# Optimization experiments

Hardware: AMD Instinct MI355X
Metric: run time of the kernel (lower is better)

Reference implementation:

```python
import jax, jax.numpy as jnp
import numpy as np

N_NODES = 100000
N_EDGES = 625000
D_IN = 128
D_OUT = 128


def setup_inputs() -> dict:
    key = jax.random.key(0)
    k1, k2, k3, k4, k5 = jax.random.split(key, 5)
    feature = jax.random.normal(k1, (N_NODES, D_IN), dtype=jnp.float32)
    W = jax.random.normal(k2, (D_OUT, D_IN), dtype=jnp.float32) * (1.0 / np.sqrt(D_IN))
    b = jax.random.normal(k3, (D_OUT,), dtype=jnp.float32) * 0.01
    src = jax.random.randint(k4, (N_EDGES,), 0, N_NODES, dtype=jnp.int64)
    dst = jax.random.randint(k5, (N_EDGES,), 0, N_NODES, dtype=jnp.int64)
    return {"feature": feature, "W": W, "b": b, "src": src, "dst": dst}


def reference(feature, W, b, src, dst):
    # copy_src: gather source-node features along edges -> [E, D_IN]
    msg = feature[src]
    # mean reduce over incoming edges per destination node
    agg = jax.ops.segment_sum(msg, dst, num_segments=N_NODES)  # [N, D_IN]
    deg = jax.ops.segment_sum(jnp.ones((dst.shape[0],), feature.dtype), dst,
                              num_segments=N_NODES)  # [N]
    # DGL mean leaves nodes with zero in-degree at 0
    h = jnp.where(deg[:, None] > 0, agg / jnp.maximum(deg, 1.0)[:, None], 0.0)
    # nn.Linear: h @ W.T + b
    return h @ W.T + b
```

## Files before the change

### kernel.cpp

```cpp
#include <hip/hip_runtime.h>

#define D 128
#define CAP 32

typedef __attribute__((ext_vector_type(8))) short short8;
typedef __attribute__((ext_vector_type(4))) float f32x4;

__device__ __forceinline__ unsigned short f2bf_rne(float x) {
    unsigned int u = __float_as_uint(x);
    u += 0x7fffu + ((u >> 16) & 1u);
    return (unsigned short)(u >> 16);
}

__global__ __launch_bounds__(256)
void pack_all(const float* __restrict__ feat, const float* __restrict__ W,
              ushort* __restrict__ fb, ushort* __restrict__ Wb, int n4) {
    int i = blockIdx.x * 256 + threadIdx.x;
    if (i < n4) {
        float4 v = ((const float4*)feat)[i];
        ushort4 o;
        o.x = f2bf_rne(v.x); o.y = f2bf_rne(v.y);
        o.z = f2bf_rne(v.z); o.w = f2bf_rne(v.w);
        ((ushort4*)fb)[i] = o;
    } else if (i < n4 + 32) {
        ((ushort4*)fb)[i] = make_ushort4(0, 0, 0, 0);
    } else if (i < n4 + 32 + 4096) {
        int j = i - (n4 + 32);
        float4 v = ((const float4*)W)[j];
        ushort4 o;
        o.x = f2bf_rne(v.x); o.y = f2bf_rne(v.y);
        o.z = f2bf_rne(v.z); o.w = f2bf_rne(v.w);
        ((ushort4*)Wb)[j] = o;
    }
}

__global__ __launch_bounds__(256)
void build_buckets(const int* __restrict__ src,
                   const int* __restrict__ dst,
                   int* __restrict__ cnt,
                   int* __restrict__ bucket,
                   int n_edges) {
    int e = blockIdx.x * 256 + threadIdx.x;
    if (e >= n_edges) return;
    int d = dst[e];
    int p = atomicAdd(cnt + d, 1);
    if (p < CAP) bucket[(size_t)d * CAP + p] = src[e];
}

__global__ __launch_bounds__(256)
void agg_gemm(const ushort* __restrict__ fb,
              const int* __restrict__ cnt,
              const int* __restrict__ bucket,
              const ushort* __restrict__ Wb,
              const float* __restrict__ b,
              float* __restrict__ out,
              int n_nodes) {
    __shared__ ushort hs[32 * 136];
    int t = threadIdx.x;
    int lane = t & 63;
    int wave = t >> 6;
    int nb = blockIdx.x * 32;
    int base = nb + wave * 8;

    int myc = (lane < 8) ? cnt[base + lane] : 0;

    const ushort* fbl = fb + (size_t)(lane << 1);

    for (int g = 0; g < 2; ++g) {
        int n0g = base + g * 4;
        int nA = n0g + (lane >> 5);
        int nB = n0g + 2 + (lane >> 5);
        int idsA = bucket[(size_t)nA * CAP + (lane & 31)];
        int idsB = bucket[(size_t)nB * CAP + (lane & 31)];
        int d0 = __shfl(myc, g * 4 + 0);
        int d1 = __shfl(myc, g * 4 + 1);
        int d2 = __shfl(myc, g * 4 + 2);
        int d3 = __shfl(myc, g * 4 + 3);
        int m0 = d0 < CAP ? d0 : CAP;
        int m1 = d1 < CAP ? d1 : CAP;
        int m2 = d2 < CAP ? d2 : CAP;
        int m3 = d3 < CAP ? d3 : CAP;
        int mA = (lane < 32) ? m0 : m1;
        int mB = (lane < 32) ? m2 : m3;
        idsA = ((lane & 31) < mA) ? idsA : n_nodes;
        idsB = ((lane & 31) < mB) ? idsB : n_nodes;
        int mm01 = m0 > m1 ? m0 : m1;
        int mm23 = m2 > m3 ? m2 : m3;
        int mmax = mm01 > mm23 ? mm01 : mm23;

        float ax0 = 0, ay0 = 0, ax1 = 0, ay1 = 0;
        float ax2 = 0, ay2 = 0, ax3 = 0, ay3 = 0;

        for (int j = 0; j < mmax; j += 8) {
            unsigned int v0[8], v1[8], v2[8], v3[8];
#pragma unroll
            for (int i = 0; i < 8; ++i) {
                int s0 = __shfl(idsA, j + i);
                int s1 = __shfl(idsA, 32 + j + i);
                int s2 = __shfl(idsB, j + i);
                int s3 = __shfl(idsB, 32 + j + i);
                v0[i] = *(const unsigned int*)(fbl + (size_t)s0 * D);
                v1[i] = *(const unsigned int*)(fbl + (size_t)s1 * D);
                v2[i] = *(const unsigned int*)(fbl + (size_t)s2 * D);
                v3[i] = *(const unsigned int*)(fbl + (size_t)s3 * D);
            }
#pragma unroll
            for (int i = 0; i < 8; ++i) {
                ax0 += __uint_as_float(v0[i] << 16); ay0 += __uint_as_float(v0[i] & 0xffff0000u);
                ax1 += __uint_as_float(v1[i] << 16); ay1 += __uint_as_float(v1[i] & 0xffff0000u);
                ax2 += __uint_as_float(v2[i] << 16); ay2 += __uint_as_float(v2[i] & 0xffff0000u);
                ax3 += __uint_as_float(v3[i] << 16); ay3 += __uint_as_float(v3[i] & 0xffff0000u);
            }
        }

        float i0 = d0 > 0 ? 1.0f / (float)d0 : 0.0f;
        float i1 = d1 > 0 ? 1.0f / (float)d1 : 0.0f;
        float i2 = d2 > 0 ? 1.0f / (float)d2 : 0.0f;
        float i3 = d3 > 0 ? 1.0f / (float)d3 : 0.0f;
        unsigned int* hsu = (unsigned int*)hs;
        int r0 = wave * 8 + g * 4;
        hsu[(r0 + 0) * 68 + lane] = ((unsigned int)f2bf_rne(ay0 * i0) << 16) | f2bf_rne(ax0 * i0);
        hsu[(r0 + 1) * 68 + lane] = ((unsigned int)f2bf_rne(ay1 * i1) << 16) | f2bf_rne(ax1 * i1);
        hsu[(r0 + 2) * 68 + lane] = ((unsigned int)f2bf_rne(ay2 * i2) << 16) | f2bf_rne(ax2 * i2);
        hsu[(r0 + 3) * 68 + lane] = ((unsigned int)f2bf_rne(ay3 * i3) << 16) | f2bf_rne(ax3 * i3);
    }
    __syncthreads();

    int mt = wave & 1;
    int nh = wave >> 1;
    int lane16 = lane & 15;
    int lq = lane >> 4;

    f32x4 acc[4] = {{0,0,0,0},{0,0,0,0},{0,0,0,0},{0,0,0,0}};
#pragma unroll
    for (int ks = 0; ks < 4; ++ks) {
        short8 afrg = *(const short8*)&hs[(mt * 16 + lane16) * 136 + ks * 32 + lq * 8];
#pragma unroll
        for (int tt = 0; tt < 4; ++tt) {
            short8 bfrg = *(const short8*)&Wb[(size_t)(nh * 64 + tt * 16 + lane16) * D + ks * 32 + lq * 8];
            acc[tt] = __builtin_amdgcn_mfma_f32_16x16x32_bf16(afrg, bfrg, acc[tt], 0, 0, 0);
        }
    }

#pragma unroll
    for (int tt = 0; tt < 4; ++tt) {
        int o = nh * 64 + tt * 16 + lane16;
        float bb = b[o];
        int node = nb + mt * 16 + lq * 4;
#pragma unroll
        for (int r = 0; r < 4; ++r) {
            out[(size_t)(node + r) * D + o] = acc[tt][r] + bb;
        }
    }
}

extern "C" void kernel_launch(void* const* d_in, const int* in_sizes, int n_in,
                              void* d_out, int out_size, void* d_ws, size_t ws_size,
                              hipStream_t stream) {
    const float* feat = (const float*)d_in[0];
    const float* W    = (const float*)d_in[1];
    const float* bia  = (const float*)d_in[2];
    const int* src = (const int*)d_in[3];
    const int* dst = (const int*)d_in[4];
    float* out = (float*)d_out;

    int n_nodes = in_sizes[0] / D;
    int n_edges = in_sizes[3];

    size_t off = 0;
    auto alloc = [&](size_t bytes) { size_t p = off; off = (off + bytes + 4095) & ~(size_t)4095; return p; };
    size_t cnt_off    = alloc((size_t)n_nodes * sizeof(int));
    size_t bucket_off = alloc((size_t)n_nodes * CAP * sizeof(int));
    size_t wb_off     = alloc((size_t)D * D * sizeof(ushort));
    size_t fb_off     = alloc((size_t)(n_nodes + 1) * D * sizeof(ushort));

    int*    cnt    = (int*)((char*)d_ws + cnt_off);
    int*    bucket = (int*)((char*)d_ws + bucket_off);
    ushort* Wb     = (ushort*)((char*)d_ws + wb_off);
    ushort* fb     = (ushort*)((char*)d_ws + fb_off);

    int n4 = n_nodes * (D / 4);
    int G  = n4 + 32 + (D * D / 4);

    hipMemsetAsync(cnt, 0, (size_t)n_nodes * sizeof(int), stream);
    pack_all<<<(G + 255) / 256, 256, 0, stream>>>(feat, W, fb, Wb, n4);
    build_buckets<<<(n_edges + 255) / 256, 256, 0, stream>>>(src, dst, cnt, bucket, n_edges);
    agg_gemm<<<n_nodes / 32, 256, 0, stream>>>(fb, cnt, bucket, Wb, bia, out, n_nodes);
}
```

Measured before the change: 190.7 us.

## Fuse pack and bucket kernels; gather 8 nodes per wave with 8-byte loads

Merges the bf16 packing kernel and the edge-bucketing kernel into one launch, with a block-index split between the two jobs. This removes one kernel launch and lets the two memory-bound phases overlap. The aggregation loop is reorganised so each half-wave handles four nodes at once over all 8 nodes per wave. Each lane now loads 8 bytes (4 bf16) per neighbour instead of 4, halving the gather instructions, and the results are written to shared memory as uint2. The cost is more accumulator registers, and all 8 nodes in a wave now iterate to the wave's maximum degree instead of the maximum of each group of 4.

```diff
diff --git a/kernel.cpp b/kernel.cpp
--- a/kernel.cpp
+++ b/kernel.cpp
@@ -12,10 +12,27 @@
     return (unsigned short)(u >> 16);
 }
 
+__device__ __forceinline__ unsigned int pack_bf2(float x, float y) {
+    return ((unsigned int)f2bf_rne(y) << 16) | (unsigned int)f2bf_rne(x);
+}
+
 __global__ __launch_bounds__(256)
-void pack_all(const float* __restrict__ feat, const float* __restrict__ W,
-              ushort* __restrict__ fb, ushort* __restrict__ Wb, int n4) {
-    int i = blockIdx.x * 256 + threadIdx.x;
+void pack_build(const float* __restrict__ feat, const float* __restrict__ W,
+                ushort* __restrict__ fb, ushort* __restrict__ Wb,
+                const int* __restrict__ src, const int* __restrict__ dst,
+                int* __restrict__ cnt, int* __restrict__ bucket,
+                int n4, int n_edges, int edgeBlocks) {
+    int bx = blockIdx.x;
+    if (bx < edgeBlocks) {
+        int e = bx * 256 + threadIdx.x;
+        if (e < n_edges) {
+            int d = dst[e];
+            int p = atomicAdd(cnt + d, 1);
+            if (p < CAP) bucket[(size_t)d * CAP + p] = src[e];
+        }
+        return;
+    }
+    int i = (bx - edgeBlocks) * 256 + threadIdx.x;
     if (i < n4) {
         float4 v = ((const float4*)feat)[i];
         ushort4 o;
@@ -35,19 +52,6 @@
 }
 
 __global__ __launch_bounds__(256)
-void build_buckets(const int* __restrict__ src,
-                   const int* __restrict__ dst,
-                   int* __restrict__ cnt,
-                   int* __restrict__ bucket,
-                   int n_edges) {
-    int e = blockIdx.x * 256 + threadIdx.x;
-    if (e >= n_edges) return;
-    int d = dst[e];
-    int p = atomicAdd(cnt + d, 1);
-    if (p < CAP) bucket[(size_t)d * CAP + p] = src[e];
-}
-
-__global__ __launch_bounds__(256)
 void agg_gemm(const ushort* __restrict__ fb,
               const int* __restrict__ cnt,
               const int* __restrict__ bucket,
@@ -62,68 +66,90 @@
     int nb = blockIdx.x * 32;
     int base = nb + wave * 8;
 
+    int hi = lane >> 5;
+    int l31 = lane & 31;
+    int half32 = lane & 32;
+
     int myc = (lane < 8) ? cnt[base + lane] : 0;
 
-    const ushort* fbl = fb + (size_t)(lane << 1);
-
-    for (int g = 0; g < 2; ++g) {
-        int n0g = base + g * 4;
-        int nA = n0g + (lane >> 5);
-        int nB = n0g + 2 + (lane >> 5);
-        int idsA = bucket[(size_t)nA * CAP + (lane & 31)];
-        int idsB = bucket[(size_t)nB * CAP + (lane & 31)];
-        int d0 = __shfl(myc, g * 4 + 0);
-        int d1 = __shfl(myc, g * 4 + 1);
-        int d2 = __shfl(myc, g * 4 + 2);
-        int d3 = __shfl(myc, g * 4 + 3);
-        int m0 = d0 < CAP ? d0 : CAP;
-        int m1 = d1 < CAP ? d1 : CAP;
-        int m2 = d2 < CAP ? d2 : CAP;
-        int m3 = d3 < CAP ? d3 : CAP;
-        int mA = (lane < 32) ? m0 : m1;
-        int mB = (lane < 32) ? m2 : m3;
-        idsA = ((lane & 31) < mA) ? idsA : n_nodes;
-        idsB = ((lane & 31) < mB) ? idsB : n_nodes;
-        int mm01 = m0 > m1 ? m0 : m1;
-        int mm23 = m2 > m3 ? m2 : m3;
-        int mmax = mm01 > mm23 ? mm01 : mm23;
-
-        float ax0 = 0, ay0 = 0, ax1 = 0, ay1 = 0;
-        float ax2 = 0, ay2 = 0, ax3 = 0, ay3 = 0;
-
-        for (int j = 0; j < mmax; j += 8) {
-            unsigned int v0[8], v1[8], v2[8], v3[8];
-#pragma unroll
-            for (int i = 0; i < 8; ++i) {
-                int s0 = __shfl(idsA, j + i);
-                int s1 = __shfl(idsA, 32 + j + i);
-                int s2 = __shfl(idsB, j + i);
-                int s3 = __shfl(idsB, 32 + j + i);
-                v0[i] = *(const unsigned int*)(fbl + (size_t)s0 * D);
-                v1[i] = *(const unsigned int*)(fbl + (size_t)s1 * D);
-                v2[i] = *(const unsigned int*)(fbl + (size_t)s2 * D);
-                v3[i] = *(const unsigned int*)(fbl + (size_t)s3 * D);
-            }
-#pragma unroll
-            for (int i = 0; i < 8; ++i) {
-                ax0 += __uint_as_float(v0[i] << 16); ay0 += __uint_as_float(v0[i] & 0xffff0000u);
-                ax1 += __uint_as_float(v1[i] << 16); ay1 += __uint_as_float(v1[i] & 0xffff0000u);
-                ax2 += __uint_as_float(v2[i] << 16); ay2 += __uint_as_float(v2[i] & 0xffff0000u);
-                ax3 += __uint_as_float(v3[i] << 16); ay3 += __uint_as_float(v3[i] & 0xffff0000u);
-            }
-        }
-
-        float i0 = d0 > 0 ? 1.0f / (float)d0 : 0.0f;
-        float i1 = d1 > 0 ? 1.0f / (float)d1 : 0.0f;
-        float i2 = d2 > 0 ? 1.0f / (float)d2 : 0.0f;
-        float i3 = d3 > 0 ? 1.0f / (float)d3 : 0.0f;
-        unsigned int* hsu = (unsigned int*)hs;
-        int r0 = wave * 8 + g * 4;
-        hsu[(r0 + 0) * 68 + lane] = ((unsigned int)f2bf_rne(ay0 * i0) << 16) | f2bf_rne(ax0 * i0);
-        hsu[(r0 + 1) * 68 + lane] = ((unsigned int)f2bf_rne(ay1 * i1) << 16) | f2bf_rne(ax1 * i1);
-        hsu[(r0 + 2) * 68 + lane] = ((unsigned int)f2bf_rne(ay2 * i2) << 16) | f2bf_rne(ax2 * i2);
-        hsu[(r0 + 3) * 68 + lane] = ((unsigned int)f2bf_rne(ay3 * i3) << 16) | f2bf_rne(ax3 * i3);
-    }
+    unsigned int so = ((unsigned int)hi << 7) + (unsigned int)l31;
+    const int* bkt = bucket + (size_t)base * CAP;
+    int ids0 = bkt[ 0 + so];
+    int ids1 = bkt[32 + so];
+    int ids2 = bkt[64 + so];
+    int ids3 = bkt[96 + so];
+
+    int d0 = __shfl(myc, 0), d1 = __shfl(myc, 1), d2 = __shfl(myc, 2), d3 = __shfl(myc, 3);
+    int d4 = __shfl(myc, 4), d5 = __shfl(myc, 5), d6 = __shfl(myc, 6), d7 = __shfl(myc, 7);
+    int c0 = min(d0, CAP), c1 = min(d1, CAP), c2 = min(d2, CAP), c3 = min(d3, CAP);
+    int c4 = min(d4, CAP), c5 = min(d5, CAP), c6 = min(d6, CAP), c7 = min(d7, CAP);
+
+    int ms0 = hi ? c4 : c0;
+    int ms1 = hi ? c5 : c1;
+    int ms2 = hi ? c6 : c2;
+    int ms3 = hi ? c7 : c3;
+    ids0 = (l31 < ms0) ? ids0 : n_nodes;
+    ids1 = (l31 < ms1) ? ids1 : n_nodes;
+    ids2 = (l31 < ms2) ? ids2 : n_nodes;
+    ids3 = (l31 < ms3) ? ids3 : n_nodes;
+
+    int mm01 = c0 > c1 ? c0 : c1;
+    int mm23 = c2 > c3 ? c2 : c3;
+    int mm45 = c4 > c5 ? c4 : c5;
+    int mm67 = c6 > c7 ? c6 : c7;
+    int mmA = mm01 > mm23 ? mm01 : mm23;
+    int mmB = mm45 > mm67 ? mm45 : mm67;
+    int mmax = mmA > mmB ? mmA : mmB;
+
+    float a00=0,a01=0,a02=0,a03=0;
+    float a10=0,a11=0,a12=0,a13=0;
+    float a20=0,a21=0,a22=0,a23=0;
+    float a30=0,a31=0,a32=0,a33=0;
+
+    const char* fbb = (const char*)fb;
+    unsigned int colb = (unsigned int)l31 * 8u;
+
+    for (int j = 0; j < mmax; j += 4) {
+        uint2 v0[4], v1[4], v2[4], v3[4];
+#pragma unroll
+        for (int i = 0; i < 4; ++i) {
+            int sl = half32 + j + i;
+            unsigned int r0 = (unsigned int)__shfl(ids0, sl);
+            unsigned int r1 = (unsigned int)__shfl(ids1, sl);
+            unsigned int r2 = (unsigned int)__shfl(ids2, sl);
+            unsigned int r3 = (unsigned int)__shfl(ids3, sl);
+            v0[i] = *(const uint2*)(fbb + ((r0 << 8) + colb));
+            v1[i] = *(const uint2*)(fbb + ((r1 << 8) + colb));
+            v2[i] = *(const uint2*)(fbb + ((r2 << 8) + colb));
+            v3[i] = *(const uint2*)(fbb + ((r3 << 8) + colb));
+        }
+#pragma unroll
+        for (int i = 0; i < 4; ++i) {
+            a00 += __uint_as_float(v0[i].x << 16); a01 += __uint_as_float(v0[i].x & 0xffff0000u);
+            a02 += __uint_as_float(v0[i].y << 16); a03 += __uint_as_float(v0[i].y & 0xffff0000u);
+            a10 += __uint_as_float(v1[i].x << 16); a11 += __uint_as_float(v1[i].x & 0xffff0000u);
+            a12 += __uint_as_float(v1[i].y << 16); a13 += __uint_as_float(v1[i].y & 0xffff0000u);
+            a20 += __uint_as_float(v2[i].x << 16); a21 += __uint_as_float(v2[i].x & 0xffff0000u);
+            a22 += __uint_as_float(v2[i].y << 16); a23 += __uint_as_float(v2[i].y & 0xffff0000u);
+            a30 += __uint_as_float(v3[i].x << 16); a31 += __uint_as_float(v3[i].x & 0xffff0000u);
+            a32 += __uint_as_float(v3[i].y << 16); a33 += __uint_as_float(v3[i].y & 0xffff0000u);
+        }
+    }
+
+    float invc = (myc > 0) ? 1.0f / (float)myc : 0.0f;
+    int selidx = half32 >> 3;
+    float inv0 = __shfl(invc, 0 + selidx);
+    float inv1 = __shfl(invc, 1 + selidx);
+    float inv2 = __shfl(invc, 2 + selidx);
+    float inv3 = __shfl(invc, 3 + selidx);
+
+    unsigned int* hsu = (unsigned int*)hs;
+    int r0 = wave * 8 + hi * 4;
+    int cu = l31 * 2;
+    *(uint2*)&hsu[(r0 + 0) * 68 + cu] = make_uint2(pack_bf2(a00*inv0, a01*inv0), pack_bf2(a02*inv0, a03*inv0));
+    *(uint2*)&hsu[(r0 + 1) * 68 + cu] = make_uint2(pack_bf2(a10*inv1, a11*inv1), pack_bf2(a12*inv1, a13*inv1));
+    *(uint2*)&hsu[(r0 + 2) * 68 + cu] = make_uint2(pack_bf2(a20*inv2, a21*inv2), pack_bf2(a22*inv2, a23*inv2));
+    *(uint2*)&hsu[(r0 + 3) * 68 + cu] = make_uint2(pack_bf2(a30*inv3, a31*inv3), pack_bf2(a32*inv3, a33*inv3));
     __syncthreads();
 
     int mt = wave & 1;
@@ -182,8 +208,11 @@
     int n4 = n_nodes * (D / 4);
     int G  = n4 + 32 + (D * D / 4);
 
+    int edgeBlocks = (n_edges + 255) / 256;
+    int packBlocks = (G + 255) / 256;
+
     hipMemsetAsync(cnt, 0, (size_t)n_nodes * sizeof(int), stream);
-    pack_all<<<(G + 255) / 256, 256, 0, stream>>>(feat, W, fb, Wb, n4);
-    build_buckets<<<(n_edges + 255) / 256, 256, 0, stream>>>(src, dst, cnt, bucket, n_edges);
+    pack_build<<<edgeBlocks + packBlocks, 256, 0, stream>>>(feat, W, fb, Wb, src, dst,
+                                                            cnt, bucket, n4, n_edges, edgeBlocks);
     agg_gemm<<<n_nodes / 32, 256, 0, stream>>>(fb, cnt, bucket, Wb, bia, out, n_nodes);
 }
```

Result: faster. 185.8 us (-2.6%).
